# Kernel optimization log

Hardware: AMD Instinct MI355X
Metric: run time of the kernel (lower is better)

The kernel has to match this reference:

```python
import jax, jax.numpy as jnp
import numpy as np

B_GR = 128    # graphs per batch
N0 = 512      # nodes per graph before pooling
E_PER = 4096  # edges per graph (kept static; pooled-away edges get weight 0)
H = 128       # hidden
F = 128       # num_features (== hidden)
C = 10        # num_classes
K_HOP = 3     # Jacobi polynomial order (hop_num)
A_J, B_J = 1.0, 1.0
EPS = 1e-5


def _bn(h, g, b):
    # training-mode BatchNorm1d: batch stats, biased variance
    m = jnp.mean(h, 0)
    v = jnp.mean((h - m) ** 2, 0)
    return (h - m) * jax.lax.rsqrt(v + EPS) * g + b


def _forward(x, convW, convb, bnW, bnB, bn7W, bn7B, attW, theta,
             lin1W, lin1b, lin2W, lin2b, lin3W, lin3b, src, dst):
    w = jnp.ones((src.shape[0],), x.dtype)  # edge weights; 0 => filtered edge
    n = N0
    h = x
    reads = []
    for i in range(5):
        N = B_GR * n
        # symmetric GCN normalization with self loops on the weighted graph
        deg = jax.ops.segment_sum(w, dst, num_segments=N) + 1.0
        dinv = jax.lax.rsqrt(deg)
        enorm = dinv[src] * dinv[dst] * w   # per-edge norm [E]
        snorm = dinv * dinv                 # self-loop norm [N]
        prop = lambda m_: jax.ops.segment_sum(enorm[:, None] * m_[src], dst, num_segments=N) + m_ * snorm[:, None]
        pvec = lambda v_: jax.ops.segment_sum(enorm * v_[src], dst, num_segments=N) + v_ * snorm
        # GCNConv -> BN -> ReLU
        h = prop(h @ convW[i]) + convb[i]
        h = jax.nn.relu(_bn(h, bnW[i], bnB[i]))
        # JacobiPool: Jacobi-polynomial diffusion of attention scores
        s0 = h @ attW[i]                    # [N]
        polys = [s0, 0.5 * ((A_J - B_J) * s0 + (A_J + B_J + 2.0) * pvec(s0))]
        for kk in range(2, K_HOP + 1):
            c0 = 2 * kk * (kk + A_J + B_J) * (2 * kk + A_J + B_J - 2)
            c1 = (2 * kk + A_J + B_J - 1) * (2 * kk + A_J + B_J) * (2 * kk + A_J + B_J - 2)
            c2 = (2 * kk + A_J + B_J - 1) * (A_J * A_J - B_J * B_J)
            c3 = 2 * (kk + A_J - 1) * (kk + B_J - 1) * (2 * kk + A_J + B_J)
            polys.append((c1 * pvec(polys[-1]) + c2 * polys[-1] - c3 * polys[-2]) / c0)
        score = sum(theta[i, j] * polys[j] for j in range(K_HOP + 1))
        # top-k node selection per graph (ratio 0.5 -> static k)
        k = n // 2
        _, idx = jax.lax.top_k(score.reshape(B_GR, n), k)
        sel = (idx + (jnp.arange(B_GR) * n)[:, None]).reshape(-1)  # global node ids [B*k]
        h = h[sel] * jnp.tanh(score[sel])[:, None]
        # remap/filter edges to surviving nodes (masked, static edge count)
        new_id = jnp.full((N,), -1, jnp.int32).at[sel].set(jnp.arange(B_GR * k, dtype=jnp.int32))
        ns, nd = new_id[src], new_id[dst]
        valid = (ns >= 0) & (nd >= 0) & (w > 0)
        w = valid.astype(x.dtype)
        src = jnp.where(valid, ns, 0)
        dst = jnp.where(valid, nd, 0)
        # readout: global max pool || global mean pool per graph
        xg = h.reshape(B_GR, k, H)
        reads.append(jnp.concatenate([xg.max(1), xg.mean(1)], -1))
        n = k
    g = sum(reads) / 5.0                    # [B, 2H]
    g = jax.nn.relu(_bn(g @ lin1W + lin1b, bnW[5], bnB[5]))
    g = jax.nn.relu(_bn(g @ lin2W + lin2b, bn7W, bn7B))
    return jax.nn.log_softmax(g @ lin3W + lin3b, -1)


def setup_inputs() -> dict:
    key = jax.random.key(0)
    ks = jax.random.split(key, 8)
    N = B_GR * N0
    E = B_GR * E_PER
    rng = np.random.default_rng(0)
    off = np.repeat(np.arange(B_GR, dtype=np.int32) * N0, E_PER)
    src = jnp.asarray(off + rng.integers(0, N0, E).astype(np.int32))
    dst = jnp.asarray(off + rng.integers(0, N0, E).astype(np.int32))
    s = 1.0 / np.sqrt(H)
    return {
        "x": jax.random.normal(ks[0], (N, F), jnp.float32),
        "convW": jax.random.normal(ks[1], (5, H, H), jnp.float32) * s,
        "convb": jnp.zeros((5, H), jnp.float32),
        "bnW": jnp.ones((6, H), jnp.float32),
        "bnB": jnp.zeros((6, H), jnp.float32),
        "bn7W": jnp.ones((H // 2,), jnp.float32),
        "bn7B": jnp.zeros((H // 2,), jnp.float32),
        "attW": jax.random.normal(ks[2], (5, H), jnp.float32) * s,
        "theta": jax.random.normal(ks[3], (5, K_HOP + 1), jnp.float32) * 0.5,
        "lin1W": jax.random.normal(ks[4], (2 * H, H), jnp.float32) * (1.0 / np.sqrt(2 * H)),
        "lin1b": jnp.zeros((H,), jnp.float32),
        "lin2W": jax.random.normal(ks[5], (H, H // 2), jnp.float32) * s,
        "lin2b": jnp.zeros((H // 2,), jnp.float32),
        "lin3W": jax.random.normal(ks[6], (H // 2, C), jnp.float32) * (1.0 / np.sqrt(H // 2)),
        "lin3b": jnp.zeros((C,), jnp.float32),
        "src": src,
        "dst": dst,
    }


def reference(x, convW, convb, bnW, bnB, bn7W, bn7B, attW, theta,
              lin1W, lin1b, lin2W, lin2b, lin3W, lin3b, src, dst):
    return _forward(x, convW, convb, bnW, bnB, bn7W, bn7B, attW, theta,
                    lin1W, lin1b, lin2W, lin2b, lin3W, lin3b, src, dst)
```

## Files before the change

### kernel.cpp

```cpp
#include <hip/hip_runtime.h>
#include <hip/hip_bf16.h>

#define B_GRAPH 128
#define ETOT    (128*4096)
#define N0G     (128*512)
#define HF      128
#define STSZ    2048

union IGSmem {
    float Ws[64*HF];
    struct { int cnt4[4][512]; int cur[512]; float dvl[512]; } ini;
};

__global__ __launch_bounds__(256) void k_init_gemm(
    const float* __restrict__ A, const float* __restrict__ Wg, float* __restrict__ C,
    const int* __restrict__ s_in, const int* __restrict__ d_in_,
    int2* __restrict__ csr, int2* __restrict__ rb2, float* __restrict__ dinvv,
    float* __restrict__ gacc, float* __restrict__ statsH,
    float* __restrict__ st0, float* __restrict__ st1, float* __restrict__ st2)
{
    __shared__ IGSmem sm;
    int t = threadIdx.x;
    if (blockIdx.x >= 128){
        int tx = t & 15, ty = t >> 4;
        int r0 = (blockIdx.x - 128)*128 + ty*8, c0 = tx*4;
        float acc[8][8];
        #pragma unroll
        for (int j=0;j<8;++j)
            #pragma unroll
            for (int l=0;l<8;++l) acc[j][l] = 0.f;
        for (int kh = 0; kh < 2; ++kh){
            __syncthreads();
            {
                float4* d4 = (float4*)sm.Ws;
                const float4* s4 = (const float4*)(Wg + kh*64*HF);
                #pragma unroll
                for (int i2 = 0; i2 < 8; ++i2) d4[t + i2*256] = s4[t + i2*256];
            }
            __syncthreads();
            for (int k4 = 0; k4 < 16; ++k4){
                float4 av[8];
                #pragma unroll
                for (int j=0;j<8;++j)
                    av[j] = *(const float4*)(A + (size_t)(r0+j)*HF + kh*64 + k4*4);
                #pragma unroll
                for (int kk=0; kk<4; ++kk){
                    int kl = k4*4 + kk;
                    float4 w0 = *(const float4*)(sm.Ws + kl*HF + c0);
                    float4 w1 = *(const float4*)(sm.Ws + kl*HF + c0 + 64);
                    #pragma unroll
                    for (int j=0;j<8;++j){
                        float a = reinterpret_cast<const float*>(&av[j])[kk];
                        acc[j][0] += a*w0.x; acc[j][1] += a*w0.y; acc[j][2] += a*w0.z; acc[j][3] += a*w0.w;
                        acc[j][4] += a*w1.x; acc[j][5] += a*w1.y; acc[j][6] += a*w1.z; acc[j][7] += a*w1.w;
                    }
                }
            }
        }
        #pragma unroll
        for (int j=0;j<8;++j){
            *(float4*)(C + (size_t)(r0+j)*HF + c0)      = make_float4(acc[j][0],acc[j][1],acc[j][2],acc[j][3]);
            *(float4*)(C + (size_t)(r0+j)*HF + c0 + 64) = make_float4(acc[j][4],acc[j][5],acc[j][6],acc[j][7]);
        }
    } else {
        int g = blockIdx.x;
        int wid = t >> 6;
        for (int l = t; l < 2048; l += 256) ((int*)sm.ini.cnt4)[l] = 0;
        gacc[g*256 + t] = 0.f;
        if (g == 0){
            if (t < 256){ statsH[t] = 0.f; if (t < 128) statsH[256+t] = 0.f; }
            for (int i = t; i < STSZ; i += 256){ st0[i] = 0.f; st1[i] = 0.f; st2[i] = 0.f; }
        }
        __syncthreads();
        for (int j = t; j < 4096; j += 256){
            int e = g*4096 + j;
            atomicAdd(&sm.ini.cnt4[wid][d_in_[e] & 511], 1);
        }
        __syncthreads();
        int c0 = sm.ini.cnt4[0][2*t] + sm.ini.cnt4[1][2*t] + sm.ini.cnt4[2][2*t] + sm.ini.cnt4[3][2*t];
        int c1 = sm.ini.cnt4[0][2*t+1] + sm.ini.cnt4[1][2*t+1] + sm.ini.cnt4[2][2*t+1] + sm.ini.cnt4[3][2*t+1];
        int pairsum = c0 + c1;
        sm.ini.cur[t] = pairsum;
        __syncthreads();
        for (int off = 1; off < 256; off <<= 1){
            int a = (t >= off) ? sm.ini.cur[t-off] : 0;
            __syncthreads();
            sm.ini.cur[t] += a;
            __syncthreads();
        }
        int begpair = sm.ini.cur[t] - pairsum;
        __syncthreads();
        sm.ini.cur[2*t]   = begpair;
        sm.ini.cur[2*t+1] = begpair + c0;
        sm.ini.cnt4[0][2*t]   = c0;
        sm.ini.cnt4[0][2*t+1] = c1;
        __syncthreads();
        for (int l = t; l < 512; l += 256){
            int cl = sm.ini.cnt4[0][l];
            rb2[g*512 + l] = make_int2(g*4096 + sm.ini.cur[l], cl);
            float dv = rsqrtf((float)cl + 1.f);
            sm.ini.dvl[l] = dv;
            dinvv[g*512 + l] = dv;
        }
        __syncthreads();
        for (int j = t; j < 4096; j += 256){
            int e = g*4096 + j;
            int sg = s_in[e], dl = d_in_[e] & 511;
            int p = atomicAdd(&sm.ini.cur[dl], 1);
            csr[g*4096 + (p & 4095)] = make_int2(sg, __float_as_int(sm.ini.dvl[sg & 511]));
        }
    }
}

__global__ __launch_bounds__(256) void k_prop_stats(const float* __restrict__ Y, const float* __restrict__ cb,
                                                    const int2* __restrict__ rb2, const int2* __restrict__ cp,
                                                    const float* __restrict__ dinv,
                                                    float* __restrict__ X, float* __restrict__ st,
                                                    int n, int lb, int Nn){
    __shared__ float rs[1024], rq[1024];
    int xcd = blockIdx.x & 7, c = blockIdx.x >> 3;
    int g = xcd*16 + (c >> lb);
    int m = c & ((1 << lb) - 1);
    int nd = threadIdx.x >> 5;
    int v = g*n + m*8 + nd;
    int f4 = threadIdx.x & 31;
    float dv = dinv[v];
    float4 y = *(const float4*)(Y + (size_t)v*HF + f4*4);
    float4 acc = make_float4(0.f, 0.f, 0.f, 0.f);
    int2 rb = rb2[v];
    int len = min(max(rb.y, 0), 4096);
    int e0 = rb.x, e1 = rb.x + len;
    for (int j = e0; j < e1; ++j){
        int2 e = cp[j];
        int s = e.x & (Nn - 1);
        float en = __int_as_float(e.y);
        float4 h = *(const float4*)(Y + (size_t)s*HF + f4*4);
        acc.x += en*h.x; acc.y += en*h.y; acc.z += en*h.z; acc.w += en*h.w;
    }
    int f = f4*4;
    acc.x = y.x*dv*dv + dv*acc.x + cb[f];
    acc.y = y.y*dv*dv + dv*acc.y + cb[f+1];
    acc.z = y.z*dv*dv + dv*acc.z + cb[f+2];
    acc.w = y.w*dv*dv + dv*acc.w + cb[f+3];
    *(float4*)(X + (size_t)v*HF + f) = acc;
    *(float4*)&rs[nd*HF + f] = acc;
    *(float4*)&rq[nd*HF + f] = make_float4(acc.x*acc.x, acc.y*acc.y, acc.z*acc.z, acc.w*acc.w);
    __syncthreads();
    if (threadIdx.x < 128){
        int tt = threadIdx.x;
        float s = 0.f, q = 0.f;
        #pragma unroll
        for (int j = 0; j < 8; ++j){ s += rs[j*HF + tt]; q += rq[j*HF + tt]; }
        atomicAdd(&st[xcd*256 + tt], s);
        atomicAdd(&st[xcd*256 + 128 + tt], q);
    }
}

__global__ __launch_bounds__(256) void k_score(
    const float* __restrict__ H, const float* __restrict__ stats,
    const float* __restrict__ gw, const float* __restrict__ gb,
    const float* __restrict__ aw, float* __restrict__ s0G, float invN)
{
    __shared__ float bna[128], bnb[128], awl[128];
    int t = threadIdx.x;
    if (t < 128){
        float s = 0.f, q = 0.f;
        #pragma unroll
        for (int b2 = 0; b2 < 8; ++b2){ s += stats[b2*256 + t]; q += stats[b2*256 + 128 + t]; }
        float mean = s*invN;
        float var  = q*invN - mean*mean;
        float iv   = rsqrtf(var + 1e-5f);
        bna[t] = iv*gw[t];
        bnb[t] = gb[t] - mean*iv*gw[t];
        awl[t] = aw[t];
    }
    __syncthreads();
    int v = blockIdx.x*128 + (t >> 1);
    int h = t & 1;
    const float* hp = H + (size_t)v*HF + h*64;
    float part = 0.f;
    #pragma unroll
    for (int j = 0; j < 16; ++j){
        float4 x = *(const float4*)(hp + j*4);
        int f = h*64 + j*4;
        float4 a4 = *(const float4*)&bna[f];
        float4 b4 = *(const float4*)&bnb[f];
        float4 w4 = *(const float4*)&awl[f];
        part += fmaxf(x.x*a4.x + b4.x, 0.f)*w4.x
              + fmaxf(x.y*a4.y + b4.y, 0.f)*w4.y
              + fmaxf(x.z*a4.z + b4.z, 0.f)*w4.z
              + fmaxf(x.w*a4.w + b4.w, 0.f)*w4.w;
    }
    float oth = __shfl_xor(part, 1);
    if (h == 0) s0G[v] = part + oth;
}

__global__ __launch_bounds__(256) void k_gemm_g(
    const float* __restrict__ Hsrc, const float* __restrict__ stats,
    const float* __restrict__ gw, const float* __restrict__ gb,
    const int* __restrict__ siG, const float* __restrict__ tssG,
    const float* __restrict__ Wg, float* __restrict__ C,
    float invN, int lk, int ln)
{
    __shared__ float Ws[64*HF];
    __shared__ float bna[128], bnb[128];
    int t = threadIdx.x;
    if (t < 128){
        float s = 0.f, q = 0.f;
        #pragma unroll
        for (int b2 = 0; b2 < 8; ++b2){ s += stats[b2*256 + t]; q += stats[b2*256 + 128 + t]; }
        float mean = s*invN;
        float var  = q*invN - mean*mean;
        float iv   = rsqrtf(var + 1e-5f);
        bna[t] = iv*gw[t];
        bnb[t] = gb[t] - mean*iv*gw[t];
    }
    int tx = t & 15, ty = t >> 4;
    int r0 = blockIdx.x*128 + ty*8, c0 = tx*4;
    int rbase[8]; float ts_[8];
    int nmask = (1 << ln) - 1;
    #pragma unroll
    for (int j = 0; j < 8; ++j){
        int rg = r0 + j;
        int g = rg >> lk;
        int old = siG[rg] & nmask;
        rbase[j] = ((g << ln) + old) * HF;
        ts_[j] = tssG[rg];
    }
    float acc[8][8];
    #pragma unroll
    for (int j=0;j<8;++j)
        #pragma unroll
        for (int l=0;l<8;++l) acc[j][l] = 0.f;
    for (int kh = 0; kh < 2; ++kh){
        __syncthreads();
        {
            float4* d4 = (float4*)Ws;
            const float4* s4 = (const float4*)(Wg + kh*64*HF);
            #pragma unroll
            for (int i2 = 0; i2 < 8; ++i2) d4[t + i2*256] = s4[t + i2*256];
        }
        __syncthreads();
        for (int k4 = 0; k4 < 16; ++k4){
            int fb = kh*64 + k4*4;
            float4 ba = *(const float4*)&bna[fb];
            float4 bb = *(const float4*)&bnb[fb];
            float4 av[8];
            #pragma unroll
            for (int j=0;j<8;++j){
                av[j] = *(const float4*)(Hsrc + (size_t)rbase[j] + fb);
                av[j].x = fmaxf(av[j].x*ba.x + bb.x, 0.f)*ts_[j];
                av[j].y = fmaxf(av[j].y*ba.y + bb.y, 0.f)*ts_[j];
                av[j].z = fmaxf(av[j].z*ba.z + bb.z, 0.f)*ts_[j];
                av[j].w = fmaxf(av[j].w*ba.w + bb.w, 0.f)*ts_[j];
            }
            #pragma unroll
            for (int kk=0; kk<4; ++kk){
                int kl = k4*4 + kk;
                float4 w0 = *(const float4*)(Ws + kl*HF + c0);
                float4 w1 = *(const float4*)(Ws + kl*HF + c0 + 64);
                #pragma unroll
                for (int j=0;j<8;++j){
                    float a = reinterpret_cast<const float*>(&av[j])[kk];
                    acc[j][0] += a*w0.x; acc[j][1] += a*w0.y; acc[j][2] += a*w0.z; acc[j][3] += a*w0.w;
                    acc[j][4] += a*w1.x; acc[j][5] += a*w1.y; acc[j][6] += a*w1.z; acc[j][7] += a*w1.w;
                }
            }
        }
    }
    #pragma unroll
    for (int j=0;j<8;++j){
        *(float4*)(C + (size_t)(r0+j)*HF + c0)      = make_float4(acc[j][0],acc[j][1],acc[j][2],acc[j][3]);
        *(float4*)(C + (size_t)(r0+j)*HF + c0 + 64) = make_float4(acc[j][4],acc[j][5],acc[j][6],acc[j][7]);
    }
}

struct __align__(16) PSmem {
    int2  eds[4096];
    int2  rbl[512];
    float dvv[512], p0[512], p1[512], p2[512];
    float ss[512]; int si[512]; float tss[256]; int nid[512];
    int   cnt_[256], scn[256], curN[256]; float dvn[256];
    float bna[128], bnb[128]; float red[1024];
};

__global__ __launch_bounds__(1024) void k_pool(
    const float* __restrict__ H, const float* __restrict__ stats,
    const float* __restrict__ gw, const float* __restrict__ gb,
    const float* __restrict__ th,
    const int2* __restrict__ rb2, int2* __restrict__ csr, const float* __restrict__ dinv,
    const float* __restrict__ s0G,
    float* __restrict__ gacc, int2* __restrict__ rb2n, float* __restrict__ dinvn,
    float* __restrict__ stZero, int* __restrict__ siG, float* __restrict__ tssG,
    const float* __restrict__ lin1W, const float* __restrict__ lin1b,
    float* __restrict__ t1g, float* __restrict__ statsH,
    float invN, float ca2, float cc2, float ca3, float cc3,
    int n, int last)
{
    int g = blockIdx.x, t = threadIdx.x;
    int k = n >> 1;
    __shared__ PSmem sm;

    if (t < 256) stZero[(g & 7)*256 + t] = 0.f;
    if (t < 128){
        float s = 0.f, q = 0.f;
        #pragma unroll
        for (int b2 = 0; b2 < 8; ++b2){ s += stats[b2*256 + t]; q += stats[b2*256 + 128 + t]; }
        float mean = s*invN;
        float var  = q*invN - mean*mean;
        float iv   = rsqrtf(var + 1e-5f);
        sm.bna[t] = iv*gw[t];
        sm.bnb[t] = gb[t] - mean*iv*gw[t];
    }
    for (int l = t; l < n; l += 1024){
        int2 rb = rb2[g*n + l];
        int bx = (rb.x - g*4096) & 4095;
        int by = min(max(rb.y, 0), 4096 - bx);
        sm.rbl[l] = make_int2(bx, by);
        sm.dvv[l] = dinv[g*n + l];
        sm.p0[l]  = s0G[g*n + l];
    }
    __syncthreads();
    int medg = sm.rbl[n-1].x + sm.rbl[n-1].y;
    for (int j = t; j < medg; j += 1024){
        int2 e = csr[g*4096 + j];
        sm.eds[j] = make_int2(e.x & (n-1), e.y);
    }
    __syncthreads();
    for (int l = t; l < n; l += 1024){
        int2 rc = sm.rbl[l];
        float acc = 0.f;
        for (int j = 0; j < rc.y; ++j){
            int2 e = sm.eds[rc.x + j];
            acc += __int_as_float(e.y) * sm.p0[e.x];
        }
        float dv = sm.dvv[l];
        sm.p1[l] = 2.f*(sm.p0[l]*dv*dv + dv*acc);
    }
    __syncthreads();
    for (int l = t; l < n; l += 1024){
        int2 rc = sm.rbl[l];
        float acc = 0.f;
        for (int j = 0; j < rc.y; ++j){
            int2 e = sm.eds[rc.x + j];
            acc += __int_as_float(e.y) * sm.p1[e.x];
        }
        float dv = sm.dvv[l];
        sm.p2[l] = ca2*(sm.p1[l]*dv*dv + dv*acc) + cc2*sm.p0[l];
    }
    __syncthreads();
    float t0v = th[0], t1v = th[1], t2c = th[2], t3v = th[3];
    for (int l = t; l < n; l += 1024){
        int2 rc = sm.rbl[l];
        float acc = 0.f;
        for (int j = 0; j < rc.y; ++j){
            int2 e = sm.eds[rc.x + j];
            acc += __int_as_float(e.y) * sm.p2[e.x];
        }
        float dv = sm.dvv[l];
        float tv = sm.p2[l]*dv*dv + dv*acc;
        float p3 = ca3*tv + cc3*sm.p1[l];
        sm.ss[l] = t0v*sm.p0[l] + t1v*sm.p1[l] + t2c*sm.p2[l] + t3v*p3;
    }
    __syncthreads();
    for (int l = t; l < n; l += 1024){
        float sl = sm.ss[l];
        int r = 0;
        for (int j = 0; j < n; j += 4){
            float4 s4 = *(const float4*)&sm.ss[j];
            r += (s4.x > sl) || (s4.x == sl && (j    ) < l);
            r += (s4.y > sl) || (s4.y == sl && (j + 1) < l);
            r += (s4.z > sl) || (s4.z == sl && (j + 2) < l);
            r += (s4.w > sl) || (s4.w == sl && (j + 3) < l);
        }
        if (r < k){
            sm.nid[l] = r;
            sm.si[r]  = l;
            float tv = tanhf(sl);
            sm.tss[r] = tv;
            siG[g*k + r]  = l;
            tssG[g*k + r] = tv;
        } else {
            sm.nid[l] = -1;
        }
    }
    __syncthreads();
    if (!last){
        if (t < k){
            int l = sm.si[t] & (n-1);
            int2 rc = sm.rbl[l];
            int c = 0;
            for (int j = 0; j < rc.y; ++j) c += (sm.nid[sm.eds[rc.x + j].x] >= 0);
            sm.cnt_[t] = c;
        }
        __syncthreads();
        int c = (t < 256) ? ((t < k) ? sm.cnt_[t] : 0) : 0;
        if (t < 256) sm.scn[t] = c;
        __syncthreads();
        for (int off = 1; off < 256; off <<= 1){
            int a = 0;
            if (t < 256 && t >= off) a = sm.scn[t-off];
            __syncthreads();
            if (t < 256) sm.scn[t] += a;
            __syncthreads();
        }
        if (t < k){
            int beg = sm.scn[t] - c;
            rb2n[g*k + t] = make_int2(g*4096 + beg, c);
            float dv = rsqrtf((float)c + 1.f);
            dinvn[g*k + t] = dv;
            sm.dvn[t] = dv;
            sm.curN[t] = beg;
        }
        __syncthreads();
        if (t < k){
            int l = sm.si[t] & (n-1);
            int2 rc = sm.rbl[l];
            int p = sm.curN[t];
            for (int j = 0; j < rc.y; ++j){
                int ns = sm.nid[sm.eds[rc.x + j].x];
                if (ns >= 0){ csr[g*4096 + (p & 4095)] = make_int2(g*k + ns, __float_as_int(sm.dvn[ns])); ++p; }
            }
        }
        __syncthreads();
    }
    {
        int f4 = t & 31, rl = t >> 5;
        int f = f4*4;
        float4 a4 = *(const float4*)&sm.bna[f];
        float4 b4 = *(const float4*)&sm.bnb[f];
        float4 mx = make_float4(-3.4e38f,-3.4e38f,-3.4e38f,-3.4e38f);
        float4 smv = make_float4(0.f,0.f,0.f,0.f);
        for (int r = rl; r < k; r += 32){
            int old = sm.si[r] & (n-1);
            float4 hv = *(const float4*)(H + ((size_t)g*n + old)*HF + f);
            float ts = sm.tss[r];
            float4 v;
            v.x = fmaxf(hv.x*a4.x + b4.x, 0.f)*ts;
            v.y = fmaxf(hv.y*a4.y + b4.y, 0.f)*ts;
            v.z = fmaxf(hv.z*a4.z + b4.z, 0.f)*ts;
            v.w = fmaxf(hv.w*a4.w + b4.w, 0.f)*ts;
            mx.x = fmaxf(mx.x, v.x); mx.y = fmaxf(mx.y, v.y);
            mx.z = fmaxf(mx.z, v.z); mx.w = fmaxf(mx.w, v.w);
            smv.x += v.x; smv.y += v.y; smv.z += v.z; smv.w += v.w;
        }
        float* scr = (float*)sm.eds;
        *(float4*)&scr[rl*128 + f]        = mx;
        *(float4*)&scr[4096 + rl*128 + f] = smv;
        __syncthreads();
        if (t < 128){
            float m = -3.4e38f, s = 0.f;
            #pragma unroll
            for (int j = 0; j < 32; ++j){
                m = fmaxf(m, scr[j*128 + t]);
                s += scr[4096 + j*128 + t];
            }
            gacc[g*256 + t] += m;
            gacc[g*256 + 128 + t] += s / (float)k;
        }
    }
    if (last){
        __syncthreads();
        int c = t & 127, h = t >> 7;
        float s = 0.f;
        int k0 = h*32;
        #pragma unroll
        for (int kk = 0; kk < 32; ++kk)
            s += gacc[g*256 + k0 + kk] * lin1W[(k0 + kk)*128 + c];
        sm.red[t] = s;
        __syncthreads();
        if (t < 512) sm.red[t] += sm.red[t+512];
        __syncthreads();
        if (t < 256) sm.red[t] += sm.red[t+256];
        __syncthreads();
        if (t < 128){
            float v = (sm.red[t] + sm.red[t+128]) * 0.2f + lin1b[t];
            t1g[g*128 + t] = v;
            atomicAdd(&statsH[t], v);
            atomicAdd(&statsH[128+t], v*v);
        }
    }
}

__global__ __launch_bounds__(128) void k_head2(const float* __restrict__ t1, const float* __restrict__ gw,
                                               const float* __restrict__ gb, const float* __restrict__ W2,
                                               const float* __restrict__ b2, float* __restrict__ sh,
                                               float* __restrict__ t2){
    int r = blockIdx.x, t = threadIdx.x;
    int cc = t & 63, h = t >> 6;
    __shared__ float row[128];
    __shared__ float red[128];
    {
        float mean = sh[t] * (1.f/128.f);
        float var  = sh[128+t]*(1.f/128.f) - mean*mean;
        float iv   = rsqrtf(var + 1e-5f);
        float v = (t1[r*128+t] - mean)*iv*gw[t] + gb[t];
        row[t] = fmaxf(v, 0.f);
    }
    __syncthreads();
    float s = 0.f;
    #pragma unroll
    for (int kk = 0; kk < 64; ++kk)
        s += row[h*64+kk] * W2[(h*64+kk)*64 + cc];
    red[t] = s;
    __syncthreads();
    if (h == 0){
        float v = red[cc] + red[cc+64] + b2[cc];
        t2[r*64+cc] = v;
        atomicAdd(&sh[256+cc], v);
        atomicAdd(&sh[320+cc], v*v);
    }
}
__global__ __launch_bounds__(64) void k_head3(const float* __restrict__ t2, const float* __restrict__ gw,
                                              const float* __restrict__ gb, const float* __restrict__ W3,
                                              const float* __restrict__ b3, const float* __restrict__ sh,
                                              float* __restrict__ out){
    int r = blockIdx.x, t = threadIdx.x;
    float mean = sh[256+t]*(1.f/128.f);
    float var  = sh[320+t]*(1.f/128.f) - mean*mean;
    float iv   = rsqrtf(var + 1e-5f);
    float v = fmaxf((t2[r*64+t]-mean)*iv*gw[t] + gb[t], 0.f);
    float lg[10];
    #pragma unroll
    for (int j = 0; j < 10; ++j){
        float p = v * W3[t*10 + j];
        for (int off = 32; off; off >>= 1) p += __shfl_down(p, off);
        lg[j] = p;
    }
    if (t == 0){
        float m = -3.4e38f;
        #pragma unroll
        for (int j = 0; j < 10; ++j){ lg[j] += b3[j]; m = fmaxf(m, lg[j]); }
        float se = 0.f;
        #pragma unroll
        for (int j = 0; j < 10; ++j) se += expf(lg[j] - m);
        float l = logf(se) + m;
        #pragma unroll
        for (int j = 0; j < 10; ++j) out[r*10 + j] = lg[j] - l;
    }
}

extern "C" void kernel_launch(void* const* d_in, const int* in_sizes, int n_in,
                              void* d_out, int out_size, void* d_ws, size_t ws_size,
                              hipStream_t stream){
    const float* x     = (const float*)d_in[0];
    const float* convW = (const float*)d_in[1];
    const float* convb = (const float*)d_in[2];
    const float* bnW   = (const float*)d_in[3];
    const float* bnB   = (const float*)d_in[4];
    const float* bn7W  = (const float*)d_in[5];
    const float* bn7B  = (const float*)d_in[6];
    const float* attW  = (const float*)d_in[7];
    const float* theta = (const float*)d_in[8];
    const float* lin1W = (const float*)d_in[9];
    const float* lin1b = (const float*)d_in[10];
    const float* lin2W = (const float*)d_in[11];
    const float* lin2b = (const float*)d_in[12];
    const float* lin3W = (const float*)d_in[13];
    const float* lin3b = (const float*)d_in[14];
    const int*   src0  = (const int*)d_in[15];
    const int*   dst0  = (const int*)d_in[16];

    char* base = (char*)d_ws;
    size_t off = 0;
    auto take = [&](size_t bytes) -> void* {
        void* p = base + off;
        off = (off + bytes + 255) & ~(size_t)255;
        return p;
    };
    float* bufGP = (float*)take((size_t)N0G*HF*4);
    float* bufHA = (float*)take((size_t)N0G*HF*4);
    float* bufHB = (float*)take((size_t)(N0G/2)*HF*4);
    int2*  csr_p = (int2*) take((size_t)ETOT*8);
    int2*  rb2A  = (int2*) take((size_t)N0G*8);
    int2*  rb2B  = (int2*) take((size_t)N0G*8);
    float* dinvA = (float*)take((size_t)N0G*4);
    float* dinvB = (float*)take((size_t)N0G*4);
    float* s0G   = (float*)take((size_t)N0G*4);
    int*   siG   = (int*)  take((size_t)(N0G/2)*4);
    float* tssG  = (float*)take((size_t)(N0G/2)*4);
    float* st[3];
    st[0] = (float*)take(STSZ*4);
    st[1] = (float*)take(STSZ*4);
    st[2] = (float*)take(STSZ*4);
    float* gacc  = (float*)take((size_t)B_GRAPH*256*4);
    float* t1    = (float*)take((size_t)B_GRAPH*128*4);
    float* t2    = (float*)take((size_t)B_GRAPH*64*4);
    float* statsH= (float*)take(384*4);

    auto coef = [](int kk, float& ca, float& cc){
        double a = 1.0, b = 1.0;
        double c0 = 2.0*kk*(kk+a+b)*(2.0*kk+a+b-2.0);
        double c1 = (2.0*kk+a+b-1.0)*(2.0*kk+a+b)*(2.0*kk+a+b-2.0);
        double c3 = 2.0*(kk+a-1.0)*(kk+b-1.0)*(2.0*kk+a+b);
        ca = (float)(c1/c0); cc = (float)(-c3/c0);
    };
    float ca2, cc2, ca3, cc3;
    coef(2, ca2, cc2);
    coef(3, ca3, cc3);

    k_init_gemm<<<128 + 512, 256, 0, stream>>>(x, convW, bufGP,
                                               src0, dst0, csr_p, rb2A, dinvA,
                                               gacc, statsH, st[0], st[1], st[2]);
    k_prop_stats<<<N0G/8, 256, 0, stream>>>(bufGP, convb, rb2A, csr_p, dinvA, bufHA, st[0], 512, 6, N0G);

    float* G = bufGP + (size_t)4*1024*1024;

    for (int i = 0; i < 5; ++i){
        int n = 512 >> i;
        int kk = n >> 1;
        int Nn = B_GRAPH*n;
        float invN = 1.0f/(float)Nn;
        int2*  rb_cur = (i & 1) ? rb2B : rb2A;
        int2*  rb_nxt = (i & 1) ? rb2A : rb2B;
        float* dv_cur = (i & 1) ? dinvB : dinvA;
        float* dv_nxt = (i & 1) ? dinvA : dinvB;
        float* Hcur = (i & 1) ? bufHB : bufHA;
        float* Hnxt = (i & 1) ? bufHA : bufHB;

        k_score<<<Nn/128, 256, 0, stream>>>(Hcur, st[i % 3], bnW + i*HF, bnB + i*HF, attW + i*HF,
                                            s0G, invN);
        k_pool<<<B_GRAPH, 1024, 0, stream>>>(Hcur, st[i % 3], bnW + i*HF, bnB + i*HF,
                                             theta + i*4, rb_cur, csr_p, dv_cur, s0G,
                                             gacc, rb_nxt, dv_nxt,
                                             st[(i + 1) % 3], siG, tssG,
                                             lin1W, lin1b, t1, statsH,
                                             invN, ca2, cc2, ca3, cc3, n, (i == 4) ? 1 : 0);
        if (i < 4){
            int wnext = i + 1;
            int rows = B_GRAPH * kk;
            int lk = 8 - i;
            int ln = 9 - i;
            k_gemm_g<<<rows/128, 256, 0, stream>>>(Hcur, st[i % 3], bnW + i*HF, bnB + i*HF,
                                                   siG, tssG, convW + (size_t)wnext*HF*HF, G,
                                                   invN, lk, ln);
            int lbn = (kk == 256) ? 5 : (kk == 128) ? 4 : (kk == 64) ? 3 : 2;
            k_prop_stats<<<rows/8, 256, 0, stream>>>(G, convb + wnext*HF, rb_nxt, csr_p, dv_nxt,
                                                     Hnxt, st[(i + 1) % 3], kk, lbn, rows);
        }
    }

    k_head2<<<B_GRAPH, 128, 0, stream>>>(t1, bnW + 5*HF, bnB + 5*HF, lin2W, lin2b, statsH, t2);
    k_head3<<<B_GRAPH, 64, 0, stream>>>(t2, bn7W, bn7B, lin3W, lin3b, statsH, (float*)d_out);
}
```

Before: 427.9 us.

## Stage per-graph feature slices in LDS for GCN propagation and widen histogram privatization

```diff
diff --git a/kernel.cpp b/kernel.cpp
--- a/kernel.cpp
+++ b/kernel.cpp
@@ -9,7 +9,7 @@
 
 union IGSmem {
     float Ws[64*HF];
-    struct { int cnt4[4][512]; int cur[512]; float dvl[512]; } ini;
+    struct { int cnt8[8][512]; int cur[512]; float dvl[512]; } ini;
 };
 
 __global__ __launch_bounds__(256) void k_init_gemm(
@@ -64,8 +64,8 @@
         }
     } else {
         int g = blockIdx.x;
-        int wid = t >> 6;
-        for (int l = t; l < 2048; l += 256) ((int*)sm.ini.cnt4)[l] = 0;
+        int wid = t >> 5;
+        for (int l = t; l < 4096; l += 256) ((int*)sm.ini.cnt8)[l] = 0;
         gacc[g*256 + t] = 0.f;
         if (g == 0){
             if (t < 256){ statsH[t] = 0.f; if (t < 128) statsH[256+t] = 0.f; }
@@ -74,11 +74,12 @@
         __syncthreads();
         for (int j = t; j < 4096; j += 256){
             int e = g*4096 + j;
-            atomicAdd(&sm.ini.cnt4[wid][d_in_[e] & 511], 1);
-        }
-        __syncthreads();
-        int c0 = sm.ini.cnt4[0][2*t] + sm.ini.cnt4[1][2*t] + sm.ini.cnt4[2][2*t] + sm.ini.cnt4[3][2*t];
-        int c1 = sm.ini.cnt4[0][2*t+1] + sm.ini.cnt4[1][2*t+1] + sm.ini.cnt4[2][2*t+1] + sm.ini.cnt4[3][2*t+1];
+            atomicAdd(&sm.ini.cnt8[wid][d_in_[e] & 511], 1);
+        }
+        __syncthreads();
+        int c0 = 0, c1 = 0;
+        #pragma unroll
+        for (int w = 0; w < 8; ++w){ c0 += sm.ini.cnt8[w][2*t]; c1 += sm.ini.cnt8[w][2*t+1]; }
         int pairsum = c0 + c1;
         sm.ini.cur[t] = pairsum;
         __syncthreads();
@@ -92,11 +93,11 @@
         __syncthreads();
         sm.ini.cur[2*t]   = begpair;
         sm.ini.cur[2*t+1] = begpair + c0;
-        sm.ini.cnt4[0][2*t]   = c0;
-        sm.ini.cnt4[0][2*t+1] = c1;
+        sm.ini.cnt8[0][2*t]   = c0;
+        sm.ini.cnt8[0][2*t+1] = c1;
         __syncthreads();
         for (int l = t; l < 512; l += 256){
-            int cl = sm.ini.cnt4[0][l];
+            int cl = sm.ini.cnt8[0][l];
             rb2[g*512 + l] = make_int2(g*4096 + sm.ini.cur[l], cl);
             float dv = rsqrtf((float)cl + 1.f);
             sm.ini.dvl[l] = dv;
@@ -109,6 +110,83 @@
             int p = atomicAdd(&sm.ini.cur[dl], 1);
             csr[g*4096 + (p & 4095)] = make_int2(sg, __float_as_int(sm.ini.dvl[sg & 511]));
         }
+    }
+}
+
+template<int NN>
+__global__ __launch_bounds__(512) void k_prop_lds(
+    const float* __restrict__ Y, const float* __restrict__ cb,
+    const int2* __restrict__ rb2, const int2* __restrict__ cp,
+    const float* __restrict__ dinv, float* __restrict__ X, float* __restrict__ st)
+{
+    constexpr int TP = 512 / NN;
+    constexpr int FQ = 8 / TP;
+    __shared__ float4 ly[NN * 8];
+    int b = blockIdx.x;
+    int g = b >> 2, q = b & 3;
+    int t = threadIdx.x;
+    const float4* Y4 = (const float4*)Y + (size_t)g*NN*32 + q*8;
+    for (int i = t; i < NN*8; i += 512){
+        int row = i >> 3, slot = i & 7;
+        ly[row*8 + ((slot + row) & 7)] = Y4[(size_t)row*32 + slot];
+    }
+    __syncthreads();
+    int r   = t & (NN - 1);
+    int sub = t / NN;
+    int S0  = sub * FQ;
+    int vg  = g*NN + r;
+    float dv = dinv[vg];
+    int2 rb = rb2[vg];
+    int e0  = (rb.x - g*4096) & 4095;
+    int len = min(max(rb.y, 0), 4096 - e0);
+    const int2* cpg = cp + g*4096 + e0;
+    float4 acc[FQ];
+    #pragma unroll
+    for (int s = 0; s < FQ; ++s) acc[s] = make_float4(0.f,0.f,0.f,0.f);
+    for (int j = 0; j < len; ++j){
+        int2 e = cpg[j];
+        int c = e.x & (NN - 1);
+        float en = __int_as_float(e.y);
+        #pragma unroll
+        for (int s = 0; s < FQ; ++s){
+            float4 h = ly[c*8 + ((S0 + s + c) & 7)];
+            acc[s].x += en*h.x; acc[s].y += en*h.y; acc[s].z += en*h.z; acc[s].w += en*h.w;
+        }
+    }
+    const float4* cb4 = (const float4*)cb + q*8;
+    float4* X4 = (float4*)X + q*8;
+    #pragma unroll
+    for (int s = 0; s < FQ; ++s){
+        float4 y = ly[r*8 + ((S0 + s + r) & 7)];
+        float4 cbv = cb4[S0 + s];
+        acc[s].x = y.x*dv*dv + dv*acc[s].x + cbv.x;
+        acc[s].y = y.y*dv*dv + dv*acc[s].y + cbv.y;
+        acc[s].z = y.z*dv*dv + dv*acc[s].z + cbv.z;
+        acc[s].w = y.w*dv*dv + dv*acc[s].w + cbv.w;
+        X4[(size_t)vg*32 + S0 + s] = acc[s];
+    }
+    __syncthreads();
+    float* lf = (float*)ly;
+    #pragma unroll
+    for (int s = 0; s < FQ; ++s) *(float4*)&lf[r*32 + (S0 + s)*4] = acc[s];
+    __syncthreads();
+    float ssum = 0.f, qsum = 0.f;
+    {
+        int col = t & 31, grp = t >> 5;
+        for (int rr = grp; rr < NN; rr += 16){
+            float v = lf[rr*32 + col];
+            ssum += v; qsum += v*v;
+        }
+    }
+    __syncthreads();
+    lf[t] = ssum; lf[512 + t] = qsum;
+    __syncthreads();
+    if (t < 64){
+        int col = t & 31, half = t >> 5;
+        float a = 0.f;
+        #pragma unroll
+        for (int i = 0; i < 16; ++i) a += lf[half*512 + i*32 + col];
+        atomicAdd(&st[(b & 7)*256 + half*128 + q*32 + col], a);
     }
 }
 
@@ -602,7 +680,7 @@
     k_init_gemm<<<128 + 512, 256, 0, stream>>>(x, convW, bufGP,
                                                src0, dst0, csr_p, rb2A, dinvA,
                                                gacc, statsH, st[0], st[1], st[2]);
-    k_prop_stats<<<N0G/8, 256, 0, stream>>>(bufGP, convb, rb2A, csr_p, dinvA, bufHA, st[0], 512, 6, N0G);
+    k_prop_lds<512><<<512, 512, 0, stream>>>(bufGP, convb, rb2A, csr_p, dinvA, bufHA, st[0]);
 
     float* G = bufGP + (size_t)4*1024*1024;
 
@@ -634,9 +712,14 @@
             k_gemm_g<<<rows/128, 256, 0, stream>>>(Hcur, st[i % 3], bnW + i*HF, bnB + i*HF,
                                                    siG, tssG, convW + (size_t)wnext*HF*HF, G,
                                                    invN, lk, ln);
-            int lbn = (kk == 256) ? 5 : (kk == 128) ? 4 : (kk == 64) ? 3 : 2;
-            k_prop_stats<<<rows/8, 256, 0, stream>>>(G, convb + wnext*HF, rb_nxt, csr_p, dv_nxt,
-                                                     Hnxt, st[(i + 1) % 3], kk, lbn, rows);
+            if (kk == 256){
+                k_prop_lds<256><<<512, 512, 0, stream>>>(G, convb + wnext*HF, rb_nxt, csr_p, dv_nxt,
+                                                         Hnxt, st[(i + 1) % 3]);
+            } else {
+                int lbn = (kk == 128) ? 4 : (kk == 64) ? 3 : 2;
+                k_prop_stats<<<rows/8, 256, 0, stream>>>(G, convb + wnext*HF, rb_nxt, csr_p, dv_nxt,
+                                                         Hnxt, st[(i + 1) % 3], kk, lbn, rows);
+            }
         }
     }
 
```

Measured after the change: 412.2 us. 1.04x faster.
